# Optimization experiments

Measured on AMD Instinct MI355X. Metric: run time of the kernel, lower is better.

The kernel has to match this reference:

```python
import jax, jax.numpy as jnp
import numpy as np
from jax import lax

T, N, E = 8192, 33, 64
D_IN, D_H, D_LSTM, N_CLS = 3, 64, 128, 5


def _lin(k, out_d, in_d):
    return jax.random.normal(k, (out_d, in_d), jnp.float32) / np.sqrt(in_d)


def setup_inputs() -> dict:
    key = jax.random.key(0)
    ks = jax.random.split(key, 16)
    x = jax.random.normal(ks[0], (T, N, D_IN), jnp.float32)
    edge_src = jax.random.randint(ks[1], (E,), 0, N)
    edge_dst = jax.random.randint(ks[2], (E,), 0, N)
    return {
        "x": x,
        "edge_src": edge_src,
        "edge_dst": edge_dst,
        "W_rel1": _lin(ks[3], D_H, D_IN),
        "b_rel1": jnp.zeros((D_H,), jnp.float32),
        "W_root1": _lin(ks[4], D_H, D_IN),
        "W_rel2": _lin(ks[5], D_H, D_H),
        "b_rel2": jnp.zeros((D_H,), jnp.float32),
        "W_root2": _lin(ks[6], D_H, D_H),
        "W_ih": _lin(ks[7], 4 * D_LSTM, D_H),
        "W_hh": _lin(ks[8], 4 * D_LSTM, D_LSTM),
        "b_ih": jnp.zeros((4 * D_LSTM,), jnp.float32),
        "b_hh": jnp.zeros((4 * D_LSTM,), jnp.float32),
        "W_fc": _lin(ks[9], N_CLS, D_LSTM),
        "b_fc": jnp.zeros((N_CLS,), jnp.float32),
    }


def graph_conv(x, src, dst, W_rel, b_rel, W_root):
    # PyG GraphConv (aggr='add'): lin_rel(scatter_add(x[src] -> dst)) + lin_root(x)
    msg = x[:, src, :]                              # [T, E, d]
    agg = jnp.zeros_like(x).at[:, dst, :].add(msg)  # [T, N, d]
    return agg @ W_rel.T + b_rel + x @ W_root.T     # [T, N, out]


def lstm_last_hidden(seq, W_ih, W_hh, b_ih, b_hh):
    # seq: [T, D_H]; torch gate order i, f, g, o
    def step(carry, xt):
        h, c = carry
        gates = xt @ W_ih.T + h @ W_hh.T + b_ih + b_hh  # [4*D_LSTM]
        i, f, g, o = jnp.split(gates, 4)
        c = jax.nn.sigmoid(f) * c + jax.nn.sigmoid(i) * jnp.tanh(g)
        h = jax.nn.sigmoid(o) * jnp.tanh(c)
        return (h, c), None
    init = (jnp.zeros((D_LSTM,), seq.dtype), jnp.zeros((D_LSTM,), seq.dtype))
    (hT, _), _ = lax.scan(step, init, seq)
    return hT


def reference(x, edge_src, edge_dst, W_rel1, b_rel1, W_root1, W_rel2, b_rel2,
              W_root2, W_ih, W_hh, b_ih, b_hh, W_fc, b_fc):
    h = graph_conv(x, edge_src, edge_dst, W_rel1, b_rel1, W_root1)  # [T,N,64]
    h = graph_conv(h, edge_src, edge_dst, W_rel2, b_rel2, W_root2)  # [T,N,64]
    h = jax.nn.relu(h)
    seq = h.mean(axis=1)                                            # global_mean_pool per frame -> [T,64]
    hT = lstm_last_hidden(seq, W_ih, W_hh, b_ih, b_hh)              # [128]
    return (hT @ W_fc.T + b_fc)[None, :]                            # [1, 5]
```

## Files before the change

kernel.cpp:

```cpp
#include <hip/hip_runtime.h>
#include <hip/hip_fp16.h>

#define T_LEN 8192
#define N_NODES 33
#define N_EDGES 64
#define DIM_IN 3
#define D_H 64
#define D_LSTM 128
#define N_CLS 5
#define TB 4

typedef float v2f __attribute__((ext_vector_type(2)));
typedef float v4f __attribute__((ext_vector_type(4)));

__global__ __launch_bounds__(64, 2) void gnn_proj_kernel(
    const float* __restrict__ x,
    const int*   __restrict__ esrc,
    const int*   __restrict__ edst,
    const float* __restrict__ W_rel1,
    const float* __restrict__ b_rel1,
    const float* __restrict__ W_root1,
    const float* __restrict__ W_rel2,
    const float* __restrict__ b_rel2,
    const float* __restrict__ W_root2,
    const float* __restrict__ W_ih,
    const float* __restrict__ b_ih,
    const float* __restrict__ b_hh,
    float* __restrict__ A)
{
    const int t0 = blockIdx.x * TB;
    const int j  = threadIdx.x;

    __shared__ __align__(16) float x_s[N_NODES][DIM_IN];
    __shared__ __align__(16) float agg1[N_NODES][DIM_IN];
    __shared__ __align__(16) float h1[N_NODES][D_H];
    __shared__ __align__(16) float agg2[N_NODES][D_H];
    __shared__ __align__(16) float seq_s[TB][D_H];
    __shared__ int es[N_EDGES], ed[N_EDGES];

    es[j] = esrc[j];
    ed[j] = edst[j];

    const float wr1_0 = W_rel1[j*3+0], wr1_1 = W_rel1[j*3+1], wr1_2 = W_rel1[j*3+2];
    const float wt1_0 = W_root1[j*3+0], wt1_1 = W_root1[j*3+1], wt1_2 = W_root1[j*3+2];
    const float br1 = b_rel1[j];
    const float br2 = b_rel2[j];

    float wr2[D_H], wt2[D_H];
    #pragma unroll
    for (int k = 0; k < D_H; ++k) {
        wr2[k] = W_rel2[j*D_H + k];
        wt2[k] = W_root2[j*D_H + k];
    }

    for (int tt = 0; tt < TB; ++tt) {
        const int t = t0 + tt;
        __syncthreads();

        const float* xt = x + (size_t)t * (N_NODES * DIM_IN);
        for (int i = j; i < N_NODES * DIM_IN; i += 64) x_s[0][i] = xt[i];
        __syncthreads();

        if (j < N_NODES) {
            float a0 = 0.f, a1 = 0.f, a2 = 0.f;
            for (int e = 0; e < N_EDGES; ++e) {
                if (ed[e] == j) {
                    a0 += x_s[es[e]][0];
                    a1 += x_s[es[e]][1];
                    a2 += x_s[es[e]][2];
                }
            }
            agg1[j][0] = a0; agg1[j][1] = a1; agg1[j][2] = a2;
        }
        __syncthreads();

        for (int n = 0; n < N_NODES; ++n) {
            float v = br1
                + agg1[n][0]*wr1_0 + agg1[n][1]*wr1_1 + agg1[n][2]*wr1_2
                + x_s[n][0]*wt1_0  + x_s[n][1]*wt1_1  + x_s[n][2]*wt1_2;
            h1[n][j]  = v;
            agg2[n][j] = 0.f;
        }
        __syncthreads();

        for (int e = 0; e < N_EDGES; ++e) {
            agg2[ed[e]][j] += h1[es[e]][j];
        }
        __syncthreads();

        float seqv = 0.f;
        for (int n = 0; n < N_NODES; ++n) {
            const float4* ag4 = (const float4*)agg2[n];
            const float4* h4  = (const float4*)h1[n];
            float acc0 = br2, acc1 = 0.f, acc2 = 0.f, acc3 = 0.f;
            #pragma unroll
            for (int k4 = 0; k4 < D_H/4; ++k4) {
                float4 av = ag4[k4];
                float4 hv = h4[k4];
                acc0 += av.x * wr2[4*k4+0] + hv.x * wt2[4*k4+0];
                acc1 += av.y * wr2[4*k4+1] + hv.y * wt2[4*k4+1];
                acc2 += av.z * wr2[4*k4+2] + hv.z * wt2[4*k4+2];
                acc3 += av.w * wr2[4*k4+3] + hv.w * wt2[4*k4+3];
            }
            float acc = (acc0 + acc1) + (acc2 + acc3);
            seqv += fmaxf(acc, 0.f);
        }
        seq_s[tt][j] = seqv * (1.0f / 33.0f);
    }
    __syncthreads();

    #pragma unroll
    for (int m = 0; m < 8; ++m) {
        const int o = m * 64 + j;
        const float bias = b_ih[o] + b_hh[o];
        const float4* w4 = (const float4*)(W_ih + (size_t)o * D_H);
        float acc[TB];
        #pragma unroll
        for (int tt = 0; tt < TB; ++tt) acc[tt] = bias;
        #pragma unroll
        for (int k4 = 0; k4 < D_H/4; ++k4) {
            float4 wv = w4[k4];
            #pragma unroll
            for (int tt = 0; tt < TB; ++tt) {
                const float4* s4 = (const float4*)seq_s[tt];
                float4 sv = s4[k4];
                acc[tt] += sv.x*wv.x + sv.y*wv.y + sv.z*wv.z + sv.w*wv.w;
            }
        }
        #pragma unroll
        for (int tt = 0; tt < TB; ++tt) {
            A[((size_t)(t0 + tt) * 128 + (o & 127)) * 4 + (o >> 7)] = acc[tt];
        }
    }
}


#define CVTPK(D,S0,S1) \
  "v_cvt_f16_f32 v190, v" #S0 "\n\t" \
  "v_cvt_f16_f32 v191, v" #S1 "\n\t" \
  "v_and_b32 v190, 0xffff, v190\n\t" \
  "v_lshlrev_b32 v191, 16, v191\n\t" \
  "v_or_b32 v" #D ", v190, v191\n\t"

#define ROWPACK(D0,D1,D2,D3,D4,D5,D6,D7,D8,D9,D10,D11,D12,D13,D14,D15) \
  CVTPK(D0,128,129) CVTPK(D1,130,131) CVTPK(D2,132,133) CVTPK(D3,134,135) \
  CVTPK(D4,136,137) CVTPK(D5,138,139) CVTPK(D6,140,141) CVTPK(D7,142,143) \
  CVTPK(D8,144,145) CVTPK(D9,146,147) CVTPK(D10,148,149) CVTPK(D11,150,151) \
  CVTPK(D12,152,153) CVTPK(D13,154,155) CVTPK(D14,156,157) CVTPK(D15,158,159)

#define ROWLOAD(WA) \
  "global_load_dwordx4 v[128:131], %[" #WA "], off\n\t" \
  "global_load_dwordx4 v[132:135], %[" #WA "], off offset:16\n\t" \
  "global_load_dwordx4 v[136:139], %[" #WA "], off offset:32\n\t" \
  "global_load_dwordx4 v[140:143], %[" #WA "], off offset:48\n\t" \
  "global_load_dwordx4 v[144:147], %[" #WA "], off offset:64\n\t" \
  "global_load_dwordx4 v[148:151], %[" #WA "], off offset:80\n\t" \
  "global_load_dwordx4 v[152:155], %[" #WA "], off offset:96\n\t" \
  "global_load_dwordx4 v[156:159], %[" #WA "], off offset:112\n\t" \
  "s_waitcnt vmcnt(0)\n\t"

#define DOT4(H, A,B,C,D) \
  "v_dot2_f32_f16 v160, v" #H ", v" #A ", v160\n\t" \
  "v_dot2_f32_f16 v161, v" #H ", v" #B ", v161\n\t" \
  "v_dot2_f32_f16 v162, v" #H ", v" #C ", v162\n\t" \
  "v_dot2_f32_f16 v163, v" #H ", v" #D ", v163\n\t"
#define DOT4Z(H, A,B,C,D) \
  "v_dot2_f32_f16 v160, v" #H ", v" #A ", 0\n\t" \
  "v_dot2_f32_f16 v161, v" #H ", v" #B ", 0\n\t" \
  "v_dot2_f32_f16 v162, v" #H ", v" #C ", 0\n\t" \
  "v_dot2_f32_f16 v163, v" #H ", v" #D ", 0\n\t"

#define HALF(P, PC, R0,R1,R2,R3, WOFF) \
  "v_add_u32 v190, s80, %[at]\n\t" \
  "global_load_dword v" #P ", v190, %[ab]\n\t" \
  "s_add_u32 s80, s80, 2048\n\t" \
  "s_cmp_lg_u32 s80, 0x1000000\n\t" \
  "s_cselect_b32 s80, s80, 0\n\t" \
  "ds_read_b128 v[128:131], %[rd] offset:" #R0 "\n\t" \
  "ds_read_b128 v[132:135], %[rd] offset:" #R1 "\n\t" \
  "ds_read_b128 v[136:139], %[rd] offset:" #R2 "\n\t" \
  "ds_read_b128 v[140:143], %[rd] offset:" #R3 "\n\t" \
  "s_waitcnt lgkmcnt(2)\n\t" \
  DOT4Z(128, 0,16,32,48) \
  DOT4(129, 1,17,33,49) \
  DOT4(130, 2,18,34,50) \
  DOT4(131, 3,19,35,51) \
  DOT4(132, 4,20,36,52) \
  DOT4(133, 5,21,37,53) \
  DOT4(134, 6,22,38,54) \
  DOT4(135, 7,23,39,55) \
  "s_waitcnt lgkmcnt(0)\n\t" \
  DOT4(136, 8,24,40,56) \
  DOT4(137, 9,25,41,57) \
  DOT4(138, 10,26,42,58) \
  DOT4(139, 11,27,43,59) \
  DOT4(140, 12,28,44,60) \
  DOT4(141, 13,29,45,61) \
  DOT4(142, 14,30,46,62) \
  DOT4(143, 15,31,47,63) \
   \
  "v_mov_b32_dpp v184, v160 quad_perm:[2,3,0,1] row_mask:0xf bank_mask:0xf\n\t" \
  "v_mov_b32_dpp v185, v161 quad_perm:[2,3,0,1] row_mask:0xf bank_mask:0xf\n\t" \
  "v_mov_b32_dpp v186, v162 quad_perm:[2,3,0,1] row_mask:0xf bank_mask:0xf\n\t" \
  "v_mov_b32_dpp v187, v163 quad_perm:[2,3,0,1] row_mask:0xf bank_mask:0xf\n\t" \
  "v_add_f32 v160, v160, v184\n\t" \
  "v_add_f32 v161, v161, v185\n\t" \
  "v_add_f32 v162, v162, v186\n\t" \
  "v_add_f32 v163, v163, v187\n\t" \
  "v_cndmask_b32 v184, v160, v162, %[mb1]\n\t" \
  "v_cndmask_b32 v185, v161, v163, %[mb1]\n\t" \
  "s_nop 1\n\t" \
  "v_mov_b32_dpp v186, v184 quad_perm:[1,0,3,2] row_mask:0xf bank_mask:0xf\n\t" \
  "v_mov_b32_dpp v187, v185 quad_perm:[1,0,3,2] row_mask:0xf bank_mask:0xf\n\t" \
  "v_add_f32 v184, v184, v186\n\t" \
  "v_add_f32 v185, v185, v187\n\t" \
  "v_cndmask_b32 v184, v184, v185, %[mb0]\n\t"    \
  "s_waitcnt vmcnt(1)\n\t" \
  "v_add_f32 v184, v184, v" #PC "\n\t" \
   \
  "v_mul_f32 v186, %[m1], v184\n\t" \
  "v_exp_f32 v186, v186\n\t" \
  "s_nop 1\n\t" \
  "v_add_f32 v186, 1.0, v186\n\t" \
  "v_rcp_f32 v186, v186\n\t" \
  "s_nop 1\n\t" \
  "v_fma_f32 v186, v186, %[sc], %[ad]\n\t" \
  "s_nop 1\n\t" \
   \
  "v_mov_b32_dpp v176, v186 quad_perm:[0,0,0,0] row_mask:0xf bank_mask:0xf\n\t" \
  "v_mov_b32_dpp v177, v186 quad_perm:[1,1,1,1] row_mask:0xf bank_mask:0xf\n\t" \
  "v_mov_b32_dpp v179, v186 quad_perm:[2,2,2,2] row_mask:0xf bank_mask:0xf\n\t" \
  "v_mov_b32_dpp v178, v186 quad_perm:[3,3,3,3] row_mask:0xf bank_mask:0xf\n\t" \
   \
  "v_mul_f32 v180, v176, v179\n\t" \
  "v_fma_f32 v181, v177, v181, v180\n\t" \
   \
  "v_mul_f32 v182, s88, v181\n\t" \
  "v_exp_f32 v182, v182\n\t" \
  "s_nop 1\n\t" \
  "v_add_f32 v182, 1.0, v182\n\t" \
  "v_rcp_f32 v182, v182\n\t" \
  "s_nop 1\n\t" \
  "v_fma_f32 v182, v182, 2.0, -1.0\n\t" \
  "v_mul_f32 v183, v178, v182\n\t" \
  "v_cvt_f16_f32 v183, v183\n\t" \
   \
  "s_and_saveexec_b64 s[84:85], s[82:83]\n\t" \
  "ds_write_b16 %[wr], v183 offset:" #WOFF "\n\t" \
  "s_mov_b64 exec, s[84:85]\n\t" \
  "s_waitcnt lgkmcnt(0)\n\t" \
  "s_barrier\n\t"

__global__ __launch_bounds__(512, 2)
__attribute__((amdgpu_waves_per_eu(2, 2)))
void lstm_kernel(
    const float* __restrict__ A,
    const float* __restrict__ W_hh,
    const float* __restrict__ W_fc,
    const float* __restrict__ b_fc,
    float* __restrict__ out)
{
    const int tid  = threadIdx.x;
    const int wave = tid >> 6;
    const int kq   = tid & 3;
    const int idx  = (tid >> 2) & 15;
    const int q    = wave * 16 + idx;
    const int kbase = kq * 32;

    __shared__ __align__(16) float h_s[2][64];

    if (tid < 128) ((float*)h_s)[tid] = 0.f;
    __syncthreads();

    const unsigned long long wai = (unsigned long long)(uintptr_t)(W_hh + (size_t)q         * D_LSTM + kbase);
    const unsigned long long waf = (unsigned long long)(uintptr_t)(W_hh + (size_t)(128 + q) * D_LSTM + kbase);
    const unsigned long long wag = (unsigned long long)(uintptr_t)(W_hh + (size_t)(256 + q) * D_LSTM + kbase);
    const unsigned long long wao = (unsigned long long)(uintptr_t)(W_hh + (size_t)(384 + q) * D_LSTM + kbase);
    const unsigned int atid = (unsigned int)(q * 16 + kq * 4);
    const unsigned int lds0 = (unsigned int)(uintptr_t)&h_s[0][0];
    const unsigned int rd   = lds0 + (unsigned int)(kq * 16);
    const int o  = q >> 3;
    const int sl = ((o & 3) << 2) | (o >> 2);
    const unsigned int wr = lds0 + (unsigned int)(sl * 16 + (q & 7) * 2);
    const unsigned long long wm  = __ballot(kq == 0);
    const unsigned long long mb0 = __ballot(kq & 1);
    const unsigned long long mb1 = __ballot(kq & 2);
    const float m1 = (kq == 2) ? -2.8853900817779268f
                               : -1.4426950408889634f;
    const float sc = (kq == 2) ? 2.0f : 1.0f;
    const float ad = (kq == 2) ? -1.0f : 0.0f;

    asm volatile(
        "s_mov_b32 s80, 2048\n\t"
        "s_mov_b32 s86, 4096\n\t"
        "s_mov_b32 s88, 0xC038AA3B\n\t"
        "s_mov_b64 s[82:83], %[wm]\n\t"
        ROWLOAD(wai)
        ROWPACK(0,1,2,3,4,5,6,7,8,9,10,11,12,13,14,15)
        ROWLOAD(waf)
        ROWPACK(16,17,18,19,20,21,22,23,24,25,26,27,28,29,30,31)
        ROWLOAD(wag)
        ROWPACK(32,33,34,35,36,37,38,39,40,41,42,43,44,45,46,47)
        ROWLOAD(wao)
        ROWPACK(48,49,50,51,52,53,54,55,56,57,58,59,60,61,62,63)
        "global_load_dword v168, %[at], %[ab]\n\t"
        "s_waitcnt vmcnt(0)\n\t"
        "v_mov_b32 v181, 0\n\t"
        "1:\n\t"
        HALF(172, 168, 0,64,128,192, 256)
        HALF(168, 172, 256,320,384,448, 0)
        "s_sub_u32 s86, s86, 1\n\t"
        "s_cmp_lg_u32 s86, 0\n\t"
        "s_cbranch_scc1 1b\n\t"
        :
        : [wai]"v"(wai), [waf]"v"(waf), [wag]"v"(wag), [wao]"v"(wao),
          [ab]"s"(A), [at]"v"(atid), [rd]"v"(rd), [wr]"v"(wr), [wm]"s"(wm),
          [mb0]"s"(mb0), [mb1]"s"(mb1), [m1]"v"(m1), [sc]"v"(sc), [ad]"v"(ad)
        : "v0","v1","v2","v3","v4","v5","v6","v7","v8","v9",
          "v10","v11","v12","v13","v14","v15","v16","v17","v18","v19",
          "v20","v21","v22","v23","v24","v25","v26","v27","v28","v29",
          "v30","v31","v32","v33","v34","v35","v36","v37","v38","v39",
          "v40","v41","v42","v43","v44","v45","v46","v47","v48","v49",
          "v50","v51","v52","v53","v54","v55","v56","v57","v58","v59",
          "v60","v61","v62","v63","v64","v65","v66","v67","v68","v69",
          "v70","v71","v72","v73","v74","v75","v76","v77","v78","v79",
          "v80","v81","v82","v83","v84","v85","v86","v87","v88","v89",
          "v90","v91","v92","v93","v94","v95","v96","v97","v98","v99",
          "v100","v101","v102","v103","v104","v105","v106","v107","v108","v109",
          "v110","v111","v112","v113","v114","v115","v116","v117","v118","v119",
          "v120","v121","v122","v123","v124","v125","v126","v127","v128","v129",
          "v130","v131","v132","v133","v134","v135","v136","v137","v138","v139",
          "v140","v141","v142","v143","v144","v145","v146","v147","v148","v149",
          "v150","v151","v152","v153","v154","v155","v156","v157","v158","v159",
          "v160","v161","v162","v163","v164","v165","v166","v167","v168","v169",
          "v170","v171","v172","v173","v174","v175","v176","v177","v178","v179",
          "v180","v181","v182","v183","v184","v185","v186","v187","v188","v189",
          "v190","v191",
          "s80","s81","s82","s83","s84","s85","s86","s87","s88",
          "scc","memory"
    );

    __syncthreads();

    if (tid < N_CLS) {
        const __half* hh = (const __half*)&h_s[0][0];
        float acc = b_fc[tid];
        #pragma unroll
        for (int k = 0; k < D_LSTM; ++k) {
            const int o2  = k >> 3;
            const int sl2 = ((o2 & 3) << 2) | (o2 >> 2);
            acc += __half2float(hh[sl2 * 8 + (k & 7)]) * W_fc[tid * D_LSTM + k];
        }
        out[tid] = acc;
    }
}

extern "C" void kernel_launch(void* const* d_in, const int* in_sizes, int n_in,
                              void* d_out, int out_size, void* d_ws, size_t ws_size,
                              hipStream_t stream) {
    const float* x       = (const float*)d_in[0];
    const int*   esrc    = (const int*)  d_in[1];
    const int*   edst    = (const int*)  d_in[2];
    const float* W_rel1  = (const float*)d_in[3];
    const float* b_rel1  = (const float*)d_in[4];
    const float* W_root1 = (const float*)d_in[5];
    const float* W_rel2  = (const float*)d_in[6];
    const float* b_rel2  = (const float*)d_in[7];
    const float* W_root2 = (const float*)d_in[8];
    const float* W_ih    = (const float*)d_in[9];
    const float* W_hh    = (const float*)d_in[10];
    const float* b_ih    = (const float*)d_in[11];
    const float* b_hh    = (const float*)d_in[12];
    const float* W_fc    = (const float*)d_in[13];
    const float* b_fc    = (const float*)d_in[14];

    float* out = (float*)d_out;
    float* A   = (float*)d_ws;

    gnn_proj_kernel<<<T_LEN / TB, 64, 0, stream>>>(
        x, esrc, edst, W_rel1, b_rel1, W_root1,
        W_rel2, b_rel2, W_root2, W_ih, b_ih, b_hh, A);

    lstm_kernel<<<1, 512, 0, stream>>>(A, W_hh, W_fc, b_fc, out);
}
```

Before: 4.461 ms.

## Use MFMA 16x16x32 f16 for LSTM recurrent matvec instead of dot2 + DPP reductions

```diff
diff --git a/kernel.cpp b/kernel.cpp
--- a/kernel.cpp
+++ b/kernel.cpp
@@ -148,105 +148,99 @@
   CVTPK(D8,144,145) CVTPK(D9,146,147) CVTPK(D10,148,149) CVTPK(D11,150,151) \
   CVTPK(D12,152,153) CVTPK(D13,154,155) CVTPK(D14,156,157) CVTPK(D15,158,159)
 
-#define ROWLOAD(WA) \
+#define FRAGLOAD(WA) \
   "global_load_dwordx4 v[128:131], %[" #WA "], off\n\t" \
   "global_load_dwordx4 v[132:135], %[" #WA "], off offset:16\n\t" \
-  "global_load_dwordx4 v[136:139], %[" #WA "], off offset:32\n\t" \
-  "global_load_dwordx4 v[140:143], %[" #WA "], off offset:48\n\t" \
-  "global_load_dwordx4 v[144:147], %[" #WA "], off offset:64\n\t" \
-  "global_load_dwordx4 v[148:151], %[" #WA "], off offset:80\n\t" \
-  "global_load_dwordx4 v[152:155], %[" #WA "], off offset:96\n\t" \
-  "global_load_dwordx4 v[156:159], %[" #WA "], off offset:112\n\t" \
+  "global_load_dwordx4 v[136:139], %[" #WA "], off offset:128\n\t" \
+  "global_load_dwordx4 v[140:143], %[" #WA "], off offset:144\n\t" \
+  "global_load_dwordx4 v[144:147], %[" #WA "], off offset:256\n\t" \
+  "global_load_dwordx4 v[148:151], %[" #WA "], off offset:272\n\t" \
+  "global_load_dwordx4 v[152:155], %[" #WA "], off offset:384\n\t" \
+  "global_load_dwordx4 v[156:159], %[" #WA "], off offset:400\n\t" \
   "s_waitcnt vmcnt(0)\n\t"
 
-#define DOT4(H, A,B,C,D) \
-  "v_dot2_f32_f16 v160, v" #H ", v" #A ", v160\n\t" \
-  "v_dot2_f32_f16 v161, v" #H ", v" #B ", v161\n\t" \
-  "v_dot2_f32_f16 v162, v" #H ", v" #C ", v162\n\t" \
-  "v_dot2_f32_f16 v163, v" #H ", v" #D ", v163\n\t"
-#define DOT4Z(H, A,B,C,D) \
-  "v_dot2_f32_f16 v160, v" #H ", v" #A ", 0\n\t" \
-  "v_dot2_f32_f16 v161, v" #H ", v" #B ", 0\n\t" \
-  "v_dot2_f32_f16 v162, v" #H ", v" #C ", 0\n\t" \
-  "v_dot2_f32_f16 v163, v" #H ", v" #D ", 0\n\t"
-
-#define HALF(P, PC, R0,R1,R2,R3, WOFF) \
-  "v_add_u32 v190, s80, %[at]\n\t" \
-  "global_load_dword v" #P ", v190, %[ab]\n\t" \
+#define HALF(P0,P3, PC0,PC1,PC2,PC3, R0,R1,R2,R3, WOFF) \
+  "ds_read_b128 v[64:67], %[rb] offset:" #R0 "\n\t" \
+  "ds_read_b128 v[68:71], %[rb] offset:" #R1 "\n\t" \
+  "ds_read_b128 v[72:75], %[rb] offset:" #R2 "\n\t" \
+  "ds_read_b128 v[76:79], %[rb] offset:" #R3 "\n\t" \
+  "v_add_u32 v189, s80, %[at]\n\t" \
+  "global_load_dwordx4 v[" #P0 ":" #P3 "], v189, %[ab]\n\t" \
   "s_add_u32 s80, s80, 2048\n\t" \
   "s_cmp_lg_u32 s80, 0x1000000\n\t" \
   "s_cselect_b32 s80, s80, 0\n\t" \
-  "ds_read_b128 v[128:131], %[rd] offset:" #R0 "\n\t" \
-  "ds_read_b128 v[132:135], %[rd] offset:" #R1 "\n\t" \
-  "ds_read_b128 v[136:139], %[rd] offset:" #R2 "\n\t" \
-  "ds_read_b128 v[140:143], %[rd] offset:" #R3 "\n\t" \
-  "s_waitcnt lgkmcnt(2)\n\t" \
-  DOT4Z(128, 0,16,32,48) \
-  DOT4(129, 1,17,33,49) \
-  DOT4(130, 2,18,34,50) \
-  DOT4(131, 3,19,35,51) \
-  DOT4(132, 4,20,36,52) \
-  DOT4(133, 5,21,37,53) \
-  DOT4(134, 6,22,38,54) \
-  DOT4(135, 7,23,39,55) \
   "s_waitcnt lgkmcnt(0)\n\t" \
-  DOT4(136, 8,24,40,56) \
-  DOT4(137, 9,25,41,57) \
-  DOT4(138, 10,26,42,58) \
-  DOT4(139, 11,27,43,59) \
-  DOT4(140, 12,28,44,60) \
-  DOT4(141, 13,29,45,61) \
-  DOT4(142, 14,30,46,62) \
-  DOT4(143, 15,31,47,63) \
-   \
-  "v_mov_b32_dpp v184, v160 quad_perm:[2,3,0,1] row_mask:0xf bank_mask:0xf\n\t" \
-  "v_mov_b32_dpp v185, v161 quad_perm:[2,3,0,1] row_mask:0xf bank_mask:0xf\n\t" \
-  "v_mov_b32_dpp v186, v162 quad_perm:[2,3,0,1] row_mask:0xf bank_mask:0xf\n\t" \
-  "v_mov_b32_dpp v187, v163 quad_perm:[2,3,0,1] row_mask:0xf bank_mask:0xf\n\t" \
-  "v_add_f32 v160, v160, v184\n\t" \
-  "v_add_f32 v161, v161, v185\n\t" \
-  "v_add_f32 v162, v162, v186\n\t" \
-  "v_add_f32 v163, v163, v187\n\t" \
-  "v_cndmask_b32 v184, v160, v162, %[mb1]\n\t" \
-  "v_cndmask_b32 v185, v161, v163, %[mb1]\n\t" \
+   \
+  "v_mfma_f32_16x16x32_f16 v[80:83], v[0:3],   v[64:67], v[164:167]\n\t" \
+  "v_mfma_f32_16x16x32_f16 v[84:87], v[16:19], v[64:67], v[164:167]\n\t" \
+  "v_mfma_f32_16x16x32_f16 v[88:91], v[32:35], v[64:67], v[164:167]\n\t" \
+  "v_mfma_f32_16x16x32_f16 v[92:95], v[48:51], v[64:67], v[164:167]\n\t" \
+  "v_mfma_f32_16x16x32_f16 v[80:83], v[4:7],   v[68:71], v[80:83]\n\t" \
+  "v_mfma_f32_16x16x32_f16 v[84:87], v[20:23], v[68:71], v[84:87]\n\t" \
+  "v_mfma_f32_16x16x32_f16 v[88:91], v[36:39], v[68:71], v[88:91]\n\t" \
+  "v_mfma_f32_16x16x32_f16 v[92:95], v[52:55], v[68:71], v[92:95]\n\t" \
+  "v_mfma_f32_16x16x32_f16 v[80:83], v[8:11],  v[72:75], v[80:83]\n\t" \
+  "v_mfma_f32_16x16x32_f16 v[84:87], v[24:27], v[72:75], v[84:87]\n\t" \
+  "v_mfma_f32_16x16x32_f16 v[88:91], v[40:43], v[72:75], v[88:91]\n\t" \
+  "v_mfma_f32_16x16x32_f16 v[92:95], v[56:59], v[72:75], v[92:95]\n\t" \
+  "v_mfma_f32_16x16x32_f16 v[80:83], v[12:15], v[76:79], v[80:83]\n\t" \
+  "v_mfma_f32_16x16x32_f16 v[84:87], v[28:31], v[76:79], v[84:87]\n\t" \
+  "v_mfma_f32_16x16x32_f16 v[88:91], v[44:47], v[76:79], v[88:91]\n\t" \
+  "v_mfma_f32_16x16x32_f16 v[92:95], v[60:63], v[76:79], v[92:95]\n\t" \
+  "s_nop 7\n\t" \
+  "s_nop 7\n\t" \
+   \
+  "v_cndmask_b32 v184, v80, v82, %[sb1]\n\t" \
+  "v_cndmask_b32 v185, v81, v83, %[sb1]\n\t" \
+  "v_cndmask_b32 v176, v184, v185, %[sb0]\n\t" \
+  "v_cndmask_b32 v184, v84, v86, %[sb1]\n\t" \
+  "v_cndmask_b32 v185, v85, v87, %[sb1]\n\t" \
+  "v_cndmask_b32 v177, v184, v185, %[sb0]\n\t" \
+  "v_cndmask_b32 v184, v88, v90, %[sb1]\n\t" \
+  "v_cndmask_b32 v185, v89, v91, %[sb1]\n\t" \
+  "v_cndmask_b32 v178, v184, v185, %[sb0]\n\t" \
+  "v_cndmask_b32 v184, v92, v94, %[sb1]\n\t" \
+  "v_cndmask_b32 v185, v93, v95, %[sb1]\n\t" \
+  "v_cndmask_b32 v179, v184, v185, %[sb0]\n\t" \
+   \
+  "s_waitcnt vmcnt(1)\n\t" \
+  "v_add_f32 v176, v176, v" #PC0 "\n\t" \
+  "v_add_f32 v177, v177, v" #PC1 "\n\t" \
+  "v_add_f32 v178, v178, v" #PC2 "\n\t" \
+  "v_add_f32 v179, v179, v" #PC3 "\n\t" \
+   \
+  "v_mul_f32 v180, s87, v176\n\t" \
+  "v_mul_f32 v181, s87, v177\n\t" \
+  "v_mul_f32 v182, s87, v179\n\t" \
+  "v_mul_f32 v183, s88, v178\n\t" \
+  "v_exp_f32 v180, v180\n\t" \
+  "v_exp_f32 v181, v181\n\t" \
+  "v_exp_f32 v182, v182\n\t" \
+  "v_exp_f32 v183, v183\n\t" \
+  "v_add_f32 v180, 1.0, v180\n\t" \
+  "v_add_f32 v181, 1.0, v181\n\t" \
+  "v_add_f32 v182, 1.0, v182\n\t" \
+  "v_add_f32 v183, 1.0, v183\n\t" \
+  "v_rcp_f32 v183, v183\n\t" \
+  "v_rcp_f32 v180, v180\n\t" \
+  "v_rcp_f32 v181, v181\n\t" \
+  "v_rcp_f32 v182, v182\n\t" \
+  "v_add_f32 v183, v183, v183\n\t" \
+  "v_add_f32 v183, -1.0, v183\n\t" \
+  "v_mul_f32 v184, v180, v183\n\t" \
+  "v_fma_f32 v190, v181, v190, v184\n\t" \
+  "v_mul_f32 v185, s88, v190\n\t" \
+  "v_exp_f32 v185, v185\n\t" \
   "s_nop 1\n\t" \
-  "v_mov_b32_dpp v186, v184 quad_perm:[1,0,3,2] row_mask:0xf bank_mask:0xf\n\t" \
-  "v_mov_b32_dpp v187, v185 quad_perm:[1,0,3,2] row_mask:0xf bank_mask:0xf\n\t" \
-  "v_add_f32 v184, v184, v186\n\t" \
-  "v_add_f32 v185, v185, v187\n\t" \
-  "v_cndmask_b32 v184, v184, v185, %[mb0]\n\t"    \
-  "s_waitcnt vmcnt(1)\n\t" \
-  "v_add_f32 v184, v184, v" #PC "\n\t" \
-   \
-  "v_mul_f32 v186, %[m1], v184\n\t" \
-  "v_exp_f32 v186, v186\n\t" \
+  "v_add_f32 v185, 1.0, v185\n\t" \
+  "v_rcp_f32 v185, v185\n\t" \
   "s_nop 1\n\t" \
-  "v_add_f32 v186, 1.0, v186\n\t" \
-  "v_rcp_f32 v186, v186\n\t" \
-  "s_nop 1\n\t" \
-  "v_fma_f32 v186, v186, %[sc], %[ad]\n\t" \
-  "s_nop 1\n\t" \
-   \
-  "v_mov_b32_dpp v176, v186 quad_perm:[0,0,0,0] row_mask:0xf bank_mask:0xf\n\t" \
-  "v_mov_b32_dpp v177, v186 quad_perm:[1,1,1,1] row_mask:0xf bank_mask:0xf\n\t" \
-  "v_mov_b32_dpp v179, v186 quad_perm:[2,2,2,2] row_mask:0xf bank_mask:0xf\n\t" \
-  "v_mov_b32_dpp v178, v186 quad_perm:[3,3,3,3] row_mask:0xf bank_mask:0xf\n\t" \
-   \
-  "v_mul_f32 v180, v176, v179\n\t" \
-  "v_fma_f32 v181, v177, v181, v180\n\t" \
-   \
-  "v_mul_f32 v182, s88, v181\n\t" \
-  "v_exp_f32 v182, v182\n\t" \
-  "s_nop 1\n\t" \
-  "v_add_f32 v182, 1.0, v182\n\t" \
-  "v_rcp_f32 v182, v182\n\t" \
-  "s_nop 1\n\t" \
-  "v_fma_f32 v182, v182, 2.0, -1.0\n\t" \
-  "v_mul_f32 v183, v178, v182\n\t" \
-  "v_cvt_f16_f32 v183, v183\n\t" \
+  "v_fma_f32 v185, v185, 2.0, -1.0\n\t" \
+  "v_mul_f32 v188, v182, v185\n\t" \
+  "v_cvt_f16_f32 v188, v188\n\t" \
    \
   "s_and_saveexec_b64 s[84:85], s[82:83]\n\t" \
-  "ds_write_b16 %[wr], v183 offset:" #WOFF "\n\t" \
+  "ds_write_b16 %[wr], v188 offset:" #WOFF "\n\t" \
   "s_mov_b64 exec, s[84:85]\n\t" \
   "s_waitcnt lgkmcnt(0)\n\t" \
   "s_barrier\n\t"
@@ -261,61 +255,61 @@
     float* __restrict__ out)
 {
     const int tid  = threadIdx.x;
+    const int lane = tid & 63;
     const int wave = tid >> 6;
-    const int kq   = tid & 3;
-    const int idx  = (tid >> 2) & 15;
-    const int q    = wave * 16 + idx;
-    const int kbase = kq * 32;
+    const int q0   = wave * 16;
+    const int row  = lane & 15;
+    const int kb8  = (lane >> 4) * 8;
+    const int u    = q0 + 4 * (lane >> 4) + (lane & 3);
 
     __shared__ __align__(16) float h_s[2][64];
 
     if (tid < 128) ((float*)h_s)[tid] = 0.f;
     __syncthreads();
 
-    const unsigned long long wai = (unsigned long long)(uintptr_t)(W_hh + (size_t)q         * D_LSTM + kbase);
-    const unsigned long long waf = (unsigned long long)(uintptr_t)(W_hh + (size_t)(128 + q) * D_LSTM + kbase);
-    const unsigned long long wag = (unsigned long long)(uintptr_t)(W_hh + (size_t)(256 + q) * D_LSTM + kbase);
-    const unsigned long long wao = (unsigned long long)(uintptr_t)(W_hh + (size_t)(384 + q) * D_LSTM + kbase);
-    const unsigned int atid = (unsigned int)(q * 16 + kq * 4);
+    const unsigned long long wai = (unsigned long long)(uintptr_t)(W_hh + (size_t)(q0 + row)        * D_LSTM + kb8);
+    const unsigned long long waf = (unsigned long long)(uintptr_t)(W_hh + (size_t)(128 + q0 + row)  * D_LSTM + kb8);
+    const unsigned long long wag = (unsigned long long)(uintptr_t)(W_hh + (size_t)(256 + q0 + row)  * D_LSTM + kb8);
+    const unsigned long long wao = (unsigned long long)(uintptr_t)(W_hh + (size_t)(384 + q0 + row)  * D_LSTM + kb8);
+    const unsigned int atid = (unsigned int)(u * 16);
     const unsigned int lds0 = (unsigned int)(uintptr_t)&h_s[0][0];
-    const unsigned int rd   = lds0 + (unsigned int)(kq * 16);
-    const int o  = q >> 3;
-    const int sl = ((o & 3) << 2) | (o >> 2);
-    const unsigned int wr = lds0 + (unsigned int)(sl * 16 + (q & 7) * 2);
-    const unsigned long long wm  = __ballot(kq == 0);
-    const unsigned long long mb0 = __ballot(kq & 1);
-    const unsigned long long mb1 = __ballot(kq & 2);
-    const float m1 = (kq == 2) ? -2.8853900817779268f
-                               : -1.4426950408889634f;
-    const float sc = (kq == 2) ? 2.0f : 1.0f;
-    const float ad = (kq == 2) ? -1.0f : 0.0f;
+    const unsigned int rb   = lds0 + (unsigned int)((lane >> 4) * 16);
+    const unsigned int wr   = lds0 + (unsigned int)(u * 2);
+    const unsigned long long wm  = __ballot((lane & 12) == 0);
+    const unsigned long long sb0 = __ballot(lane & 1);
+    const unsigned long long sb1 = __ballot(lane & 2);
 
     asm volatile(
         "s_mov_b32 s80, 2048\n\t"
         "s_mov_b32 s86, 4096\n\t"
+        "s_mov_b32 s87, 0xBFB8AA3B\n\t"
         "s_mov_b32 s88, 0xC038AA3B\n\t"
         "s_mov_b64 s[82:83], %[wm]\n\t"
-        ROWLOAD(wai)
+        FRAGLOAD(wai)
         ROWPACK(0,1,2,3,4,5,6,7,8,9,10,11,12,13,14,15)
-        ROWLOAD(waf)
+        FRAGLOAD(waf)
         ROWPACK(16,17,18,19,20,21,22,23,24,25,26,27,28,29,30,31)
-        ROWLOAD(wag)
+        FRAGLOAD(wag)
         ROWPACK(32,33,34,35,36,37,38,39,40,41,42,43,44,45,46,47)
-        ROWLOAD(wao)
+        FRAGLOAD(wao)
         ROWPACK(48,49,50,51,52,53,54,55,56,57,58,59,60,61,62,63)
-        "global_load_dword v168, %[at], %[ab]\n\t"
+        "v_mov_b32 v164, 0\n\t"
+        "v_mov_b32 v165, 0\n\t"
+        "v_mov_b32 v166, 0\n\t"
+        "v_mov_b32 v167, 0\n\t"
+        "global_load_dwordx4 v[168:171], %[at], %[ab]\n\t"
         "s_waitcnt vmcnt(0)\n\t"
-        "v_mov_b32 v181, 0\n\t"
+        "v_mov_b32 v190, 0\n\t"
         "1:\n\t"
-        HALF(172, 168, 0,64,128,192, 256)
-        HALF(168, 172, 256,320,384,448, 0)
+        HALF(172,175, 168,169,170,171, 0,64,128,192, 256)
+        HALF(168,171, 172,173,174,175, 256,320,384,448, 0)
         "s_sub_u32 s86, s86, 1\n\t"
         "s_cmp_lg_u32 s86, 0\n\t"
         "s_cbranch_scc1 1b\n\t"
         :
         : [wai]"v"(wai), [waf]"v"(waf), [wag]"v"(wag), [wao]"v"(wao),
-          [ab]"s"(A), [at]"v"(atid), [rd]"v"(rd), [wr]"v"(wr), [wm]"s"(wm),
-          [mb0]"s"(mb0), [mb1]"s"(mb1), [m1]"v"(m1), [sc]"v"(sc), [ad]"v"(ad)
+          [ab]"s"(A), [at]"v"(atid), [rb]"v"(rb), [wr]"v"(wr), [wm]"s"(wm),
+          [sb0]"s"(sb0), [sb1]"s"(sb1)
         : "v0","v1","v2","v3","v4","v5","v6","v7","v8","v9",
           "v10","v11","v12","v13","v14","v15","v16","v17","v18","v19",
           "v20","v21","v22","v23","v24","v25","v26","v27","v28","v29",
@@ -347,9 +341,7 @@
         float acc = b_fc[tid];
         #pragma unroll
         for (int k = 0; k < D_LSTM; ++k) {
-            const int o2  = k >> 3;
-            const int sl2 = ((o2 & 3) << 2) | (o2 >> 2);
-            acc += __half2float(hh[sl2 * 8 + (k & 7)]) * W_fc[tid * D_LSTM + k];
+            acc += __half2float(hh[k]) * W_fc[tid * D_LSTM + k];
         }
         out[tid] = acc;
     }
```

Result: faster. 3.876 ms (-13.1%).
